# Kernel optimization log

Measured on AMD Instinct MI355X. Metric: run time of the kernel, lower is better.

## Reference

```python
import jax, jax.numpy as jnp
import numpy as np

D, H, L, P, NQ, B, DFF = 256, 8, 4, 4, 900, 4, 1024
SHAPES = [(128, 128), (64, 64), (32, 32), (16, 16)]
S = sum(h * w for h, w in SHAPES)  # 21760
HD = D // H


def setup_inputs() -> dict:
    key = jax.random.key(0)
    ks = iter(jax.random.split(key, 32))
    r = lambda sh, s=1.0: jax.random.normal(next(ks), sh, jnp.float32) * s
    return dict(
        tgt=r((B, NQ, D)),
        query_pos=r((B, NQ, D)),
        reference_points=jax.random.uniform(next(ks), (B, NQ, L, 2), jnp.float32),
        memory=r((B, S, D)),
        in_proj_w=r((D, 3 * D), 0.02), in_proj_b=jnp.zeros(3 * D, jnp.float32),
        out_proj_w=r((D, D), 0.02), out_proj_b=jnp.zeros(D, jnp.float32),
        ln1_g=jnp.ones(D, jnp.float32), ln1_b=jnp.zeros(D, jnp.float32),
        ln2_g=jnp.ones(D, jnp.float32), ln2_b=jnp.zeros(D, jnp.float32),
        ln3_g=jnp.ones(D, jnp.float32), ln3_b=jnp.zeros(D, jnp.float32),
        vproj_w=r((D, D), 0.02), vproj_b=jnp.zeros(D, jnp.float32),
        off_w=r((D, H * L * P * 2), 0.02), off_b=r((H * L * P * 2,), 0.5),
        aw_w=r((D, H * L * P), 0.02), aw_b=jnp.zeros(H * L * P, jnp.float32),
        oproj_w=r((D, D), 0.02), oproj_b=jnp.zeros(D, jnp.float32),
        lin1_w=r((D, DFF), 0.02), lin1_b=jnp.zeros(DFF, jnp.float32),
        lin2_w=r((DFF, D), 0.02), lin2_b=jnp.zeros(D, jnp.float32),
        spatial_shapes=np.array(SHAPES, np.int32),
        mem_mask=jnp.zeros((B, S), bool),
    )


def _ln(x, g, b):
    m = jnp.mean(x, -1, keepdims=True)
    v = jnp.mean((x - m) ** 2, -1, keepdims=True)
    return (x - m) * jax.lax.rsqrt(v + 1e-5) * g + b


def reference(tgt, query_pos, reference_points, memory,
              in_proj_w, in_proj_b, out_proj_w, out_proj_b,
              ln1_g, ln1_b, ln2_g, ln2_b, ln3_g, ln3_b,
              vproj_w, vproj_b, off_w, off_b, aw_w, aw_b, oproj_w, oproj_b,
              lin1_w, lin1_b, lin2_w, lin2_b, spatial_shapes, mem_mask):
    shapes = np.asarray(spatial_shapes)  # static level shapes

    # ---- self attention (nn.MultiheadAttention, q=k=tgt+pos, v=tgt) ----
    qp = tgt + query_pos
    q = qp @ in_proj_w[:, :D] + in_proj_b[:D]
    k = qp @ in_proj_w[:, D:2 * D] + in_proj_b[D:2 * D]
    v = tgt @ in_proj_w[:, 2 * D:] + in_proj_b[2 * D:]
    split = lambda x: x.reshape(B, NQ, H, HD).transpose(0, 2, 1, 3)
    qh, kh, vh = split(q), split(k), split(v)
    att = jax.nn.softmax(jnp.einsum('bhqd,bhkd->bhqk', qh, kh) / np.sqrt(HD).astype(np.float32), -1)
    sa = jnp.einsum('bhqk,bhkd->bhqd', att, vh).transpose(0, 2, 1, 3).reshape(B, NQ, D)
    tgt = _ln(tgt + sa @ out_proj_w + out_proj_b, ln2_g, ln2_b)

    # ---- MSDeformAttn cross attention ----
    query = tgt + query_pos
    value = memory @ vproj_w + vproj_b
    value = jnp.where(mem_mask[..., None], 0.0, value).reshape(B, S, H, HD)
    off = (query @ off_w + off_b).reshape(B, NQ, H, L, P, 2)
    aw = jax.nn.softmax((query @ aw_w + aw_b).reshape(B, NQ, H, L * P), -1).reshape(B, NQ, H, L, P)
    # offset normalizer is (W_l, H_l)
    normalizer = jnp.stack([jnp.asarray(shapes[:, 1]), jnp.asarray(shapes[:, 0])], -1).astype(jnp.float32)
    loc = reference_points[:, :, None, :, None, :] + off / normalizer[None, None, None, :, None, :]

    acc = jnp.zeros((B, NQ, H, HD), tgt.dtype)
    start = 0
    bidx = jnp.arange(B)[:, None, None, None]
    hidx = jnp.arange(H)[None, None, :, None]
    for l in range(L):
        Hl, Wl = int(shapes[l, 0]), int(shapes[l, 1])
        vf = value[:, start:start + Hl * Wl]  # [B, Hl*Wl, H, HD]
        # grid_sample align_corners=False, zero padding: pixel = loc*size - 0.5
        x = loc[:, :, :, l, :, 0] * Wl - 0.5  # [B,NQ,H,P]
        y = loc[:, :, :, l, :, 1] * Hl - 0.5
        x0 = jnp.floor(x); y0 = jnp.floor(y)
        wx = x - x0; wy = y - y0
        x0i = x0.astype(jnp.int32); y0i = y0.astype(jnp.int32)

        def gather(xi, yi):
            valid = (xi >= 0) & (xi < Wl) & (yi >= 0) & (yi < Hl)
            idx = jnp.clip(yi, 0, Hl - 1) * Wl + jnp.clip(xi, 0, Wl - 1)
            g = vf[bidx, idx, hidx]  # [B,NQ,H,P,HD]
            return jnp.where(valid[..., None], g, 0.0)

        samp = (gather(x0i, y0i) * ((1 - wx) * (1 - wy))[..., None]
                + gather(x0i + 1, y0i) * (wx * (1 - wy))[..., None]
                + gather(x0i, y0i + 1) * ((1 - wx) * wy)[..., None]
                + gather(x0i + 1, y0i + 1) * (wx * wy)[..., None])
        acc = acc + (samp * aw[:, :, :, l, :, None]).sum(3)
        start += Hl * Wl

    ca = acc.reshape(B, NQ, D) @ oproj_w + oproj_b
    tgt = _ln(tgt + ca, ln1_g, ln1_b)

    # ---- FFN ----
    ff = jax.nn.relu(tgt @ lin1_w + lin1_b) @ lin2_w + lin2_b
    return _ln(tgt + ff, ln3_g, ln3_b)
```

## Files before the change

kernel.cpp:

```cpp
#include <hip/hip_runtime.h>
#include <hip/hip_bf16.h>

typedef __attribute__((ext_vector_type(8))) short bf16x8;
typedef __attribute__((ext_vector_type(4))) short bf16x4;
typedef __attribute__((ext_vector_type(4))) float f32x4;

#define DEV static __device__ __forceinline__

constexpr int Bc = 4, NQc = 900, Hc = 8, Sc = 21760;
constexpr int M1 = Bc * NQc;
constexpr int NQT = (NQc + 63) / 64;
constexpr int QT16 = (NQc + 15) / 16;
constexpr int QKo = Bc * Hc * 960 * 32;

DEV short f2bf(float f) {
  union { __hip_bfloat16 h; short s; } u;
  u.h = __float2bfloat16(f);
  return u.s;
}
DEV float bf2f(short s) {
  union { short s; __hip_bfloat16 h; } u;
  u.s = s;
  return __bfloat162float(u.h);
}

DEV void pack_body(const float* W, short* Wt, int K, int N, int t) {
  int n = t % N;
  int k4 = (t / N) * 4;
  bf16x4 o;
  o[0] = f2bf(W[(size_t)(k4 + 0) * N + n]);
  o[1] = f2bf(W[(size_t)(k4 + 1) * N + n]);
  o[2] = f2bf(W[(size_t)(k4 + 2) * N + n]);
  o[3] = f2bf(W[(size_t)(k4 + 3) * N + n]);
  *(bf16x4*)&Wt[((size_t)(k4 >> 5) * N + n) * 32 + (k4 & 31)] = o;
}

__global__ __launch_bounds__(256) void pack_all_k(
    const float* w0, short* t0, const float* w1, short* t1,
    const float* w2, short* t2, const float* w3, short* t3,
    const float* w4, short* t4, const float* w5, short* t5) {
  int t = blockIdx.x * 256 + threadIdx.x;
  if (t < 49152) pack_body(w0, t0, 256, 768, t);
  else if (t < 65536) pack_body(w1, t1, 256, 256, t - 49152);
  else if (t < 81920) pack_body(w2, t2, 256, 256, t - 65536);
  else if (t < 98304) pack_body(w3, t3, 256, 256, t - 81920);
  else if (t < 163840) pack_body(w4, t4, 256, 1024, t - 98304);
  else pack_body(w5, t5, 1024, 256, t - 163840);
}

template <int MODE, int ACT, int MT>
__global__ __launch_bounds__(256) void gemmv_k(
    const float* __restrict__ A, const float* __restrict__ A2,
    const short* __restrict__ Wt, const float* __restrict__ bias,
    void* __restrict__ Cv, float* __restrict__ C2, int M, int N, int K,
    const unsigned char* __restrict__ rowmask, const float* __restrict__ g,
    const float* __restrict__ beta, const float* __restrict__ resid,
    const float* __restrict__ qpos, float* __restrict__ out2) {
  constexpr int IT = MT / 16;
  __shared__ short As[MT * 40];
  __shared__ short Ws[256 * 40];
  const int nb = N >> 8;
  const int mb = blockIdx.x / nb, bn = blockIdx.x - mb * nb;
  const int tid = threadIdx.x;
  const int lane = tid & 63, wave = tid >> 6;
  const int l16 = lane & 15, quad = lane >> 4;
  const int sr = (MT == 64) ? (tid >> 2) : (tid >> 3);
  const int sk = (MT == 64) ? ((tid & 3) * 8) : ((tid & 7) * 4);
  const int arow = mb * MT + sr;
  const bool aval = arow < M;
  const bool useA2 = (MODE == 4) ? (bn < 2) : (A2 != nullptr);
  const float* ap = A + (size_t)arow * K + sk;
  const float* ap2 = (A2 ? A2 : A) + (size_t)arow * K + sk;
  const short* wp = Wt + (size_t)(bn * 256 + tid) * 32;
  const size_t wstep = (size_t)N * 32;
  const int KT = K >> 5;

  f32x4 acc[IT][4] = {};
  float4 pa0[2] = {}, pa1[2] = {};
  bf16x8 pw[2][4];

  auto loadA = [&](int s, int it) {
    if (aval) {
      const float* p = ap + it * 32;
      pa0[s] = *(const float4*)p;
      if constexpr (MT == 64) pa1[s] = *(const float4*)(p + 4);
      if (useA2) {
        const float* p2 = ap2 + it * 32;
        float4 q0 = *(const float4*)p2;
        pa0[s].x += q0.x; pa0[s].y += q0.y; pa0[s].z += q0.z; pa0[s].w += q0.w;
        if constexpr (MT == 64) {
          float4 q1 = *(const float4*)(p2 + 4);
          pa1[s].x += q1.x; pa1[s].y += q1.y; pa1[s].z += q1.z; pa1[s].w += q1.w;
        }
      }
    }
  };
  auto loadW = [&](int s, int it) {
    const short* p = wp + (size_t)it * wstep;
    pw[s][0] = *(const bf16x8*)(p + 0);
    pw[s][1] = *(const bf16x8*)(p + 8);
    pw[s][2] = *(const bf16x8*)(p + 16);
    pw[s][3] = *(const bf16x8*)(p + 24);
  };
  auto stage = [&](int s) {
    if constexpr (MT == 64) {
      bf16x8 t;
      t[0] = f2bf(pa0[s].x); t[1] = f2bf(pa0[s].y); t[2] = f2bf(pa0[s].z); t[3] = f2bf(pa0[s].w);
      t[4] = f2bf(pa1[s].x); t[5] = f2bf(pa1[s].y); t[6] = f2bf(pa1[s].z); t[7] = f2bf(pa1[s].w);
      *(bf16x8*)&As[sr * 40 + sk] = t;
    } else {
      bf16x4 t;
      t[0] = f2bf(pa0[s].x); t[1] = f2bf(pa0[s].y); t[2] = f2bf(pa0[s].z); t[3] = f2bf(pa0[s].w);
      *(bf16x4*)&As[sr * 40 + sk] = t;
    }
    short* wd = &Ws[tid * 40];
    *(bf16x8*)(wd + 0) = pw[s][0];
    *(bf16x8*)(wd + 8) = pw[s][1];
    *(bf16x8*)(wd + 16) = pw[s][2];
    *(bf16x8*)(wd + 24) = pw[s][3];
  };
  auto compute = [&]() {
    bf16x8 af[IT], bfr[4];
#pragma unroll
    for (int i = 0; i < IT; i++)
      af[i] = *(const bf16x8*)&As[(i * 16 + l16) * 40 + quad * 8];
#pragma unroll
    for (int j = 0; j < 4; j++)
      bfr[j] = *(const bf16x8*)&Ws[(wave * 64 + j * 16 + l16) * 40 + quad * 8];
#pragma unroll
    for (int i = 0; i < IT; i++)
#pragma unroll
      for (int j = 0; j < 4; j++)
        acc[i][j] = __builtin_amdgcn_mfma_f32_16x16x32_bf16(af[i], bfr[j], acc[i][j], 0, 0, 0);
  };

  loadA(0, 0); loadW(0, 0);
  loadA(1, 1); loadW(1, 1);
  for (int it = 0; it < KT; it += 2) {
    stage(0);
    __syncthreads();
    if (it + 2 < KT) { loadA(0, it + 2); loadW(0, it + 2); }
    compute();
    __syncthreads();
    stage(1);
    __syncthreads();
    if (it + 3 < KT) { loadA(1, it + 3); loadW(1, it + 3); }
    compute();
    __syncthreads();
  }

  if constexpr (MODE == 4) {
    short* base = (short*)Cv;
#pragma unroll
    for (int i = 0; i < IT; i++)
#pragma unroll
      for (int r = 0; r < 4; r++) {
        const int m = mb * MT + i * 16 + quad * 4 + r;
        if (m >= M) continue;
        const int b = m / NQc, q = m - b * NQc;
#pragma unroll
        for (int j = 0; j < 4; j++) {
          const int cl = wave * 64 + j * 16 + l16;
          const float v = acc[i][j][r] + bias[bn * 256 + cl];
          const int h = cl >> 5, ch = cl & 31;
          if (bn == 0) {
            base[((size_t)(b * 8 + h) * 960 + q) * 32 + ch] =
                f2bf(v * 0.17677669529663687f);
          } else if (bn == 1) {
            base[QKo + ((size_t)(b * 8 + h) * 960 + q) * 32 + ch] = f2bf(v);
          } else {
            base[2 * QKo + ((((size_t)(b * 8 + h) * 15 + (q >> 6)) * 32 + ch) * 64 + (q & 63))] = f2bf(v);
          }
        }
      }
  } else if constexpr (MODE == 0) {
#pragma unroll
    for (int i = 0; i < IT; i++)
#pragma unroll
      for (int j = 0; j < 4; j++) {
        const int cl = wave * 64 + j * 16 + l16;
        const int col = bn * 256 + cl;
        const float bb = bias[col];
#pragma unroll
        for (int r = 0; r < 4; r++) {
          const int m = mb * MT + i * 16 + quad * 4 + r;
          if (m < M) {
            float v = acc[i][j][r] + bb;
            if (ACT == 1) v = fmaxf(v, 0.f);
            ((float*)Cv)[(size_t)m * N + col] = v;
          }
        }
      }
  } else {
#pragma unroll
    for (int j = 0; j < 4; j++) {
      const int cl = wave * 64 + j * 16 + l16;
      const float bb = bias[cl];
#pragma unroll
      for (int i = 0; i < IT; i++)
#pragma unroll
        for (int r = 0; r < 4; r++) {
          const int m = mb * MT + i * 16 + quad * 4 + r;
          const float rs = (m < M) ? resid[(size_t)m * 256 + cl] : 0.f;
          acc[i][j][r] += bb + rs;
        }
    }
    float2* pr = (float2*)As;
#pragma unroll
    for (int i = 0; i < IT; i++)
#pragma unroll
      for (int r = 0; r < 4; r++) {
        float s = 0.f, q = 0.f;
#pragma unroll
        for (int j = 0; j < 4; j++) {
          s += acc[i][j][r];
          q += acc[i][j][r] * acc[i][j][r];
        }
#pragma unroll
        for (int d = 1; d < 16; d <<= 1) {
          s += __shfl_xor(s, d);
          q += __shfl_xor(q, d);
        }
        if (l16 == 0) pr[(i * 16 + quad * 4 + r) * 4 + wave] = make_float2(s, q);
      }
    __syncthreads();
#pragma unroll
    for (int i = 0; i < IT; i++)
#pragma unroll
      for (int r = 0; r < 4; r++) {
        const int ml = i * 16 + quad * 4 + r;
        float2 p0 = pr[ml * 4 + 0], p1 = pr[ml * 4 + 1];
        float2 p2 = pr[ml * 4 + 2], p3 = pr[ml * 4 + 3];
        const float sum = p0.x + p1.x + p2.x + p3.x;
        const float sq = p0.y + p1.y + p2.y + p3.y;
        const float mean = sum * (1.f / 256.f);
        const float var = sq * (1.f / 256.f) - mean * mean;
        const float rstd = rsqrtf(var + 1e-5f);
        const int m = mb * MT + ml;
        if (m < M) {
#pragma unroll
          for (int j = 0; j < 4; j++) {
            const int cl = wave * 64 + j * 16 + l16;
            const float o = (acc[i][j][r] - mean) * rstd * g[cl] + beta[cl];
            ((float*)Cv)[(size_t)m * 256 + cl] = o;
            if (out2) out2[(size_t)m * 256 + cl] = o + qpos[(size_t)m * 256 + cl];
          }
        }
      }
  }
}

__global__ __launch_bounds__(256) void gemm_val_k(
    const float* __restrict__ A, const short* __restrict__ Wt,
    const float* __restrict__ bias, short* __restrict__ Cv, int M,
    const unsigned char* __restrict__ rowmask) {
  __shared__ short As[128 * 40];
  __shared__ short Ws[256 * 40];
  const int mb = blockIdx.x;
  const int tid = threadIdx.x;
  const int lane = tid & 63, wave = tid >> 6;
  const int l16 = lane & 15, quad = lane >> 4;
  const int sr = tid >> 1, sk = (tid & 1) * 16;
  const int arow = mb * 128 + sr;
  const bool aval = arow < M;
  const float* ap = A + (size_t)arow * 256 + sk;
  const short* wp = Wt + (size_t)tid * 32;

  f32x4 acc[8][4] = {};
  float4 pa[4];
  bf16x8 pwr[4];

  auto loadA = [&](int it) {
    if (aval) {
#pragma unroll
      for (int i = 0; i < 4; i++) pa[i] = *(const float4*)(ap + it * 32 + i * 4);
    }
  };
  auto loadW = [&](int it) {
    const short* p = wp + (size_t)it * (256 * 32);
    pwr[0] = *(const bf16x8*)(p + 0);
    pwr[1] = *(const bf16x8*)(p + 8);
    pwr[2] = *(const bf16x8*)(p + 16);
    pwr[3] = *(const bf16x8*)(p + 24);
  };

  loadA(0); loadW(0);
  for (int it = 0; it < 8; ++it) {
    {
      bf16x8 t0, t1;
      t0[0] = f2bf(pa[0].x); t0[1] = f2bf(pa[0].y); t0[2] = f2bf(pa[0].z); t0[3] = f2bf(pa[0].w);
      t0[4] = f2bf(pa[1].x); t0[5] = f2bf(pa[1].y); t0[6] = f2bf(pa[1].z); t0[7] = f2bf(pa[1].w);
      t1[0] = f2bf(pa[2].x); t1[1] = f2bf(pa[2].y); t1[2] = f2bf(pa[2].z); t1[3] = f2bf(pa[2].w);
      t1[4] = f2bf(pa[3].x); t1[5] = f2bf(pa[3].y); t1[6] = f2bf(pa[3].z); t1[7] = f2bf(pa[3].w);
      *(bf16x8*)&As[sr * 40 + sk] = t0;
      *(bf16x8*)&As[sr * 40 + sk + 8] = t1;
      short* wd = &Ws[tid * 40];
      *(bf16x8*)(wd + 0) = pwr[0];
      *(bf16x8*)(wd + 8) = pwr[1];
      *(bf16x8*)(wd + 16) = pwr[2];
      *(bf16x8*)(wd + 24) = pwr[3];
    }
    __syncthreads();
    if (it + 1 < 8) { loadA(it + 1); loadW(it + 1); }
    bf16x8 af[8], bfr[4];
#pragma unroll
    for (int i = 0; i < 8; i++)
      af[i] = *(const bf16x8*)&As[(i * 16 + l16) * 40 + quad * 8];
#pragma unroll
    for (int j = 0; j < 4; j++)
      bfr[j] = *(const bf16x8*)&Ws[(wave * 64 + j * 16 + l16) * 40 + quad * 8];
#pragma unroll
    for (int i = 0; i < 8; i++)
#pragma unroll
      for (int j = 0; j < 4; j++)
        acc[i][j] = __builtin_amdgcn_mfma_f32_16x16x32_bf16(af[i], bfr[j], acc[i][j], 0, 0, 0);
    __syncthreads();
  }
#pragma unroll
  for (int i = 0; i < 8; i++)
#pragma unroll
    for (int j = 0; j < 4; j++) {
      const int cl = wave * 64 + j * 16 + l16;
      const float bb = bias[cl];
#pragma unroll
      for (int r = 0; r < 4; r++) {
        const int m = mb * 128 + i * 16 + quad * 4 + r;
        if (m < M) {
          float v = acc[i][j][r] + bb;
          if (rowmask[m]) v = 0.f;
          Cv[(size_t)m * 256 + cl] = f2bf(v);
        }
      }
    }
}

DEV void gemm32_body(const float* __restrict__ A, const float* __restrict__ W,
                     const float* __restrict__ bias, float* __restrict__ C,
                     int M, int N, int K, int bid) {
  __shared__ float Asf[16][64];
  __shared__ float Bsf[16][68];
  const int nb = N >> 6;
  const int bm = bid / nb, bn = bid % nb;
  const int tid = threadIdx.x;
  const int tm = tid >> 4, tn = tid & 15;
  float acc[4][4] = {};

  for (int k0 = 0; k0 < K; k0 += 16) {
    {
      const int m = tid >> 2, kk = (tid & 3) * 4;
      const int row = bm * 64 + m;
      float4 v = (row < M) ? *(const float4*)(A + (size_t)row * K + k0 + kk)
                           : make_float4(0.f, 0.f, 0.f, 0.f);
      Asf[kk + 0][m] = v.x; Asf[kk + 1][m] = v.y;
      Asf[kk + 2][m] = v.z; Asf[kk + 3][m] = v.w;
    }
    {
      const int kk = tid >> 4, n = (tid & 15) * 4;
      float4 v = *(const float4*)(W + (size_t)(k0 + kk) * N + bn * 64 + n);
      *(float4*)&Bsf[kk][n] = v;
    }
    __syncthreads();
#pragma unroll
    for (int kk = 0; kk < 16; kk++) {
      float a[4], b[4];
#pragma unroll
      for (int i = 0; i < 4; i++) a[i] = Asf[kk][tm * 4 + i];
#pragma unroll
      for (int j = 0; j < 4; j++) b[j] = Bsf[kk][tn * 4 + j];
#pragma unroll
      for (int i = 0; i < 4; i++)
#pragma unroll
        for (int j = 0; j < 4; j++) acc[i][j] = fmaf(a[i], b[j], acc[i][j]);
    }
    __syncthreads();
  }
#pragma unroll
  for (int i = 0; i < 4; i++) {
    const int row = bm * 64 + tm * 4 + i;
    if (row >= M) continue;
#pragma unroll
    for (int j = 0; j < 4; j++) {
      const int col = bn * 64 + tn * 4 + j;
      C[(size_t)row * N + col] = acc[i][j] + bias[col];
    }
  }
}

__global__ __launch_bounds__(256) void gemm32_offaw_k(
    const float* __restrict__ query, const float* __restrict__ off_w,
    const float* __restrict__ off_b, float* __restrict__ offb,
    const float* __restrict__ aw_w, const float* __restrict__ aw_b,
    float* __restrict__ awlin) {
  if (blockIdx.x < 228)
    gemm32_body(query, off_w, off_b, offb, M1, 256, 256, blockIdx.x);
  else
    gemm32_body(query, aw_w, aw_b, awlin, M1, 128, 256, blockIdx.x - 228);
}

__global__ __launch_bounds__(128) void attn_k(const short* __restrict__ qbf,
                                              const short* __restrict__ kbf,
                                              const short* __restrict__ vtbf,
                                              float* __restrict__ sa) {
  __shared__ short Pb[2][16 * 72];
  __shared__ float Om[2][16][32];
  __shared__ float Ml[2][16][2];
  const int bid = blockIdx.x;
  const int qt = bid % QT16, bh = bid / QT16;
  const int tid = threadIdx.x, lane = tid & 63, wave = tid >> 6;
  const int l16 = lane & 15, quad = lane >> 4;

  const int q_local = min(qt * 16 + l16, NQc - 1);
  const bf16x8 qf = *(const bf16x8*)&qbf[((size_t)bh * 960 + q_local) * 32 + quad * 8];
  const short* kb = kbf + (size_t)bh * 960 * 32;
  const short* vb = vtbf + (size_t)bh * 15 * 32 * 64;

  f32x4 o0 = {}, o1 = {};
  float mrun[4] = {-1e30f, -1e30f, -1e30f, -1e30f};
  float lrun[4] = {0.f, 0.f, 0.f, 0.f};
  short* pw = Pb[wave];

  for (int kt = wave; kt < NQT; kt += 2) {
    const int k0 = kt * 64;
    f32x4 s[4];
#pragma unroll
    for (int st = 0; st < 4; st++) {
      const int key = k0 + st * 16 + l16;
      const bf16x8 kf = *(const bf16x8*)&kb[(size_t)key * 32 + quad * 8];
      f32x4 z = {};
      s[st] = __builtin_amdgcn_mfma_f32_16x16x32_bf16(qf, kf, z, 0, 0, 0);
      if (key >= NQc) { s[st][0] = -1e30f; s[st][1] = -1e30f; s[st][2] = -1e30f; s[st][3] = -1e30f; }
    }
    float mnew[4], alpha[4];
#pragma unroll
    for (int r = 0; r < 4; r++) {
      float mx = fmaxf(fmaxf(s[0][r], s[1][r]), fmaxf(s[2][r], s[3][r]));
#pragma unroll
      for (int d = 1; d < 16; d <<= 1) mx = fmaxf(mx, __shfl_xor(mx, d));
      mnew[r] = fmaxf(mrun[r], mx);
      alpha[r] = __expf(mrun[r] - mnew[r]);
      mrun[r] = mnew[r];
    }
    float tsum[4] = {0.f, 0.f, 0.f, 0.f};
#pragma unroll
    for (int st = 0; st < 4; st++)
#pragma unroll
      for (int r = 0; r < 4; r++) {
        float p = __expf(s[st][r] - mnew[r]);
        s[st][r] = p;
        tsum[r] += p;
      }
#pragma unroll
    for (int r = 0; r < 4; r++) {
      float t = tsum[r];
#pragma unroll
      for (int d = 1; d < 16; d <<= 1) t += __shfl_xor(t, d);
      lrun[r] = lrun[r] * alpha[r] + t;
      o0[r] *= alpha[r];
      o1[r] *= alpha[r];
    }
#pragma unroll
    for (int st = 0; st < 4; st++)
#pragma unroll
      for (int r = 0; r < 4; r++)
        pw[(quad * 4 + r) * 72 + st * 16 + l16] = f2bf(s[st][r]);
    const short* vt = vb + kt * (32 * 64);
#pragma unroll
    for (int c = 0; c < 2; c++) {
      bf16x8 pf = *(const bf16x8*)&pw[l16 * 72 + c * 32 + quad * 8];
      bf16x8 vf0 = *(const bf16x8*)&vt[(size_t)l16 * 64 + c * 32 + quad * 8];
      bf16x8 vf1 = *(const bf16x8*)&vt[(size_t)(16 + l16) * 64 + c * 32 + quad * 8];
      o0 = __builtin_amdgcn_mfma_f32_16x16x32_bf16(pf, vf0, o0, 0, 0, 0);
      o1 = __builtin_amdgcn_mfma_f32_16x16x32_bf16(pf, vf1, o1, 0, 0, 0);
    }
  }
#pragma unroll
  for (int r = 0; r < 4; r++) {
    Om[wave][quad * 4 + r][l16] = o0[r];
    Om[wave][quad * 4 + r][16 + l16] = o1[r];
  }
  if (l16 == 0) {
#pragma unroll
    for (int r = 0; r < 4; r++) {
      Ml[wave][quad * 4 + r][0] = mrun[r];
      Ml[wave][quad * 4 + r][1] = lrun[r];
    }
  }
  __syncthreads();
  {
    const int q = tid >> 3;
    const int c4 = (tid & 7) * 4;
    const float m0 = Ml[0][q][0], m1 = Ml[1][q][0];
    const float M = fmaxf(m0, m1);
    const float a0 = __expf(m0 - M), a1 = __expf(m1 - M);
    const float lsum = a0 * Ml[0][q][1] + a1 * Ml[1][q][1];
    const int qg = qt * 16 + q;
    if (qg < NQc) {
      const float inv = 1.f / lsum;
      float4 o;
      o.x = (a0 * Om[0][q][c4 + 0] + a1 * Om[1][q][c4 + 0]) * inv;
      o.y = (a0 * Om[0][q][c4 + 1] + a1 * Om[1][q][c4 + 1]) * inv;
      o.z = (a0 * Om[0][q][c4 + 2] + a1 * Om[1][q][c4 + 2]) * inv;
      o.w = (a0 * Om[0][q][c4 + 3] + a1 * Om[1][q][c4 + 3]) * inv;
      const int b = bh >> 3, h = bh & 7;
      *(float4*)&sa[(size_t)(b * NQc + qg) * 256 + h * 32 + c4] = o;
    }
  }
}

__global__ __launch_bounds__(256) void sample_k(
    const float* __restrict__ awlin, const float* __restrict__ off,
    const float* __restrict__ refp, const short* __restrict__ value,
    float* __restrict__ accout) {
  const int wid = blockIdx.x * 4 + (threadIdx.x >> 6);
  const int lane = threadIdx.x & 63;
  const int bq = wid >> 3, h = wid & 7;
  const int b = bq / NQc;
  const int l16 = lane & 15;

  float wraw = awlin[(size_t)bq * 128 + h * 16 + l16];
  float mx = wraw;
#pragma unroll
  for (int d = 1; d < 16; d <<= 1) mx = fmaxf(mx, __shfl_xor(mx, d));
  float e = __expf(wraw - mx), ssum = e;
#pragma unroll
  for (int d = 1; d < 16; d <<= 1) ssum += __shfl_xor(ssum, d);
  const float wnorm = e / ssum;

  const int ch = lane & 31, sub = lane >> 5;
  float facc = 0.f;
#pragma unroll
  for (int it = 0; it < 8; it++) {
    const int pt = it * 2 + sub;
    const float w = __shfl(wnorm, pt);
    const int l = pt >> 2;
    const int W = 128 >> l;
    const int start = (l == 0) ? 0 : (l == 1) ? 16384 : (l == 2) ? 20480 : 21504;
    const float offx = off[(size_t)bq * 256 + h * 32 + pt * 2];
    const float offy = off[(size_t)bq * 256 + h * 32 + pt * 2 + 1];
    const float rx = refp[(size_t)bq * 8 + l * 2];
    const float ry = refp[(size_t)bq * 8 + l * 2 + 1];
    const float x = rx * (float)W + offx - 0.5f;
    const float y = ry * (float)W + offy - 0.5f;
    const float x0f = floorf(x), y0f = floorf(y);
    const float wx = x - x0f, wy = y - y0f;
    const int x0 = (int)x0f, y0 = (int)y0f;
    const short* vbp = value + ((size_t)b * Sc + start) * 256 + h * 32 + ch;
#pragma unroll
    for (int c4 = 0; c4 < 4; c4++) {
      const int dx = c4 & 1, dy = c4 >> 1;
      const int xi = x0 + dx, yi = y0 + dy;
      const bool valid = (xi >= 0) && (xi < W) && (yi >= 0) && (yi < W);
      const int xc = min(max(xi, 0), W - 1);
      const int yc = min(max(yi, 0), W - 1);
      const float gvv = bf2f(vbp[(size_t)(yc * W + xc) * 256]);
      const float ww = (dx ? wx : 1.f - wx) * (dy ? wy : 1.f - wy);
      facc += valid ? w * ww * gvv : 0.f;
    }
  }
  facc += __shfl_xor(facc, 32);
  if (lane < 32) accout[(size_t)bq * 256 + h * 32 + ch] = facc;
}

extern "C" void kernel_launch(void* const* d_in, const int* in_sizes, int n_in,
                              void* d_out, int out_size, void* d_ws,
                              size_t ws_size, hipStream_t stream) {
  const float* tgt = (const float*)d_in[0];
  const float* query_pos = (const float*)d_in[1];
  const float* refp = (const float*)d_in[2];
  const float* memory = (const float*)d_in[3];
  const float* in_proj_w = (const float*)d_in[4];
  const float* in_proj_b = (const float*)d_in[5];
  const float* out_proj_w = (const float*)d_in[6];
  const float* out_proj_b = (const float*)d_in[7];
  const float* ln1_g = (const float*)d_in[8];
  const float* ln1_b = (const float*)d_in[9];
  const float* ln2_g = (const float*)d_in[10];
  const float* ln2_b = (const float*)d_in[11];
  const float* ln3_g = (const float*)d_in[12];
  const float* ln3_b = (const float*)d_in[13];
  const float* vproj_w = (const float*)d_in[14];
  const float* vproj_b = (const float*)d_in[15];
  const float* off_w = (const float*)d_in[16];
  const float* off_b = (const float*)d_in[17];
  const float* aw_w = (const float*)d_in[18];
  const float* aw_b = (const float*)d_in[19];
  const float* oproj_w = (const float*)d_in[20];
  const float* oproj_b = (const float*)d_in[21];
  const float* lin1_w = (const float*)d_in[22];
  const float* lin1_b = (const float*)d_in[23];
  const float* lin2_w = (const float*)d_in[24];
  const float* lin2_b = (const float*)d_in[25];
  const unsigned char* mem_mask = (const unsigned char*)d_in[27];
  float* out = (float*)d_out;

  float* ws = (float*)d_ws;
  short* qbf = (short*)(ws + 921600);
  float* sa = ws + 3686400;
  float* tgt2 = ws + 5529600;
  float* query = ws + 6451200;
  float* offb = ws + 7372800;
  float* awlin = ws + 8294400;
  float* accb = ws + 8755200;
  float* tgt3 = ws + 9676800;
  float* ff1 = ws + 10598400;
  short* valueBf = (short*)(ws + 14284800);
  short* wbase = valueBf + 22282240;
  short* inT = wbase + 0;
  short* outT = wbase + 196608;
  short* vT = wbase + 262144;
  short* oT = wbase + 327680;
  short* lin1T = wbase + 393216;
  short* lin2T = wbase + 655360;

  pack_all_k<<<896, 256, 0, stream>>>(in_proj_w, inT, out_proj_w, outT,
                                      vproj_w, vT, oproj_w, oT,
                                      lin1_w, lin1T, lin2_w, lin2T);

  gemmv_k<4, 0, 32><<<113 * 3, 256, 0, stream>>>(
      tgt, query_pos, inT, in_proj_b, qbf, nullptr, M1, 768, 256,
      nullptr, nullptr, nullptr, nullptr, nullptr, nullptr);
  attn_k<<<Bc * Hc * QT16, 128, 0, stream>>>(qbf, qbf + QKo, qbf + 2 * QKo, sa);
  gemmv_k<3, 0, 32><<<113, 256, 0, stream>>>(
      sa, nullptr, outT, out_proj_b, tgt2, nullptr, M1, 256, 256,
      nullptr, ln2_g, ln2_b, tgt, query_pos, query);
  gemm_val_k<<<680, 256, 0, stream>>>(memory, vT, vproj_b, valueBf, Bc * Sc, mem_mask);
  gemm32_offaw_k<<<342, 256, 0, stream>>>(query, off_w, off_b, offb, aw_w, aw_b, awlin);
  sample_k<<<Bc * NQc * Hc / 4, 256, 0, stream>>>(awlin, offb, refp, valueBf, accb);
  gemmv_k<3, 0, 32><<<113, 256, 0, stream>>>(
      accb, nullptr, oT, oproj_b, tgt3, nullptr, M1, 256, 256,
      nullptr, ln1_g, ln1_b, tgt2, nullptr, nullptr);
  gemmv_k<0, 1, 64><<<57 * 4, 256, 0, stream>>>(
      tgt3, nullptr, lin1T, lin1_b, ff1, nullptr, M1, 1024, 256,
      nullptr, nullptr, nullptr, nullptr, nullptr, nullptr);
  gemmv_k<3, 0, 32><<<113, 256, 0, stream>>>(
      ff1, nullptr, lin2T, lin2_b, out, nullptr, M1, 256, 1024,
      nullptr, ln3_g, ln3_b, tgt3, nullptr, nullptr);
}
```

Measured before the change: 429.3 us.

## Drop LDS staging in value-projection GEMM, load fragments directly from global

The value-projection GEMM no longer stages A and W tiles through shared memory with barriers. Each lane loads its MFMA fragments straight from global memory into a double-buffered register pipeline. The M tile shrinks from 128 to 64 rows, doubling the grid to 1360 blocks. This removes the LDS round trips and syncthreads. In exchange the four waves now reread the same A rows from global memory or cache, and the accesses are less coalesced. The rows-in-range guard on A loads is also dropped, which relies on M dividing evenly by 64 (87040 does).

```diff
diff --git a/kernel.cpp b/kernel.cpp
--- a/kernel.cpp
+++ b/kernel.cpp
@@ -254,82 +254,77 @@
     const float* __restrict__ A, const short* __restrict__ Wt,
     const float* __restrict__ bias, short* __restrict__ Cv, int M,
     const unsigned char* __restrict__ rowmask) {
-  __shared__ short As[128 * 40];
-  __shared__ short Ws[256 * 40];
   const int mb = blockIdx.x;
   const int tid = threadIdx.x;
   const int lane = tid & 63, wave = tid >> 6;
   const int l16 = lane & 15, quad = lane >> 4;
-  const int sr = tid >> 1, sk = (tid & 1) * 16;
-  const int arow = mb * 128 + sr;
-  const bool aval = arow < M;
-  const float* ap = A + (size_t)arow * 256 + sk;
-  const short* wp = Wt + (size_t)tid * 32;
-
-  f32x4 acc[8][4] = {};
-  float4 pa[4];
-  bf16x8 pwr[4];
-
-  auto loadA = [&](int it) {
-    if (aval) {
-#pragma unroll
-      for (int i = 0; i < 4; i++) pa[i] = *(const float4*)(ap + it * 32 + i * 4);
+
+  const float* ap = A + (size_t)(mb * 64 + l16) * 256 + quad * 8;
+  const short* wp = Wt + (size_t)(wave * 64 + l16) * 32 + quad * 8;
+
+  f32x4 acc[4][4] = {};
+  float4 pa[2][4][2];
+  bf16x8 pb[2][4];
+
+  auto loadA = [&](int s, int it) {
+#pragma unroll
+    for (int i = 0; i < 4; i++) {
+      const float* p = ap + (size_t)i * (16 * 256) + it * 32;
+      pa[s][i][0] = *(const float4*)p;
+      pa[s][i][1] = *(const float4*)(p + 4);
     }
   };
-  auto loadW = [&](int it) {
-    const short* p = wp + (size_t)it * (256 * 32);
-    pwr[0] = *(const bf16x8*)(p + 0);
-    pwr[1] = *(const bf16x8*)(p + 8);
-    pwr[2] = *(const bf16x8*)(p + 16);
-    pwr[3] = *(const bf16x8*)(p + 24);
+  auto loadB = [&](int s, int it) {
+#pragma unroll
+    for (int j = 0; j < 4; j++)
+      pb[s][j] = *(const bf16x8*)(wp + (size_t)(it * 256 + j * 16) * 32);
   };
-
-  loadA(0); loadW(0);
-  for (int it = 0; it < 8; ++it) {
-    {
-      bf16x8 t0, t1;
-      t0[0] = f2bf(pa[0].x); t0[1] = f2bf(pa[0].y); t0[2] = f2bf(pa[0].z); t0[3] = f2bf(pa[0].w);
-      t0[4] = f2bf(pa[1].x); t0[5] = f2bf(pa[1].y); t0[6] = f2bf(pa[1].z); t0[7] = f2bf(pa[1].w);
-      t1[0] = f2bf(pa[2].x); t1[1] = f2bf(pa[2].y); t1[2] = f2bf(pa[2].z); t1[3] = f2bf(pa[2].w);
-      t1[4] = f2bf(pa[3].x); t1[5] = f2bf(pa[3].y); t1[6] = f2bf(pa[3].z); t1[7] = f2bf(pa[3].w);
-      *(bf16x8*)&As[sr * 40 + sk] = t0;
-      *(bf16x8*)&As[sr * 40 + sk + 8] = t1;
-      short* wd = &Ws[tid * 40];
-      *(bf16x8*)(wd + 0) = pwr[0];
-      *(bf16x8*)(wd + 8) = pwr[1];
-      *(bf16x8*)(wd + 16) = pwr[2];
-      *(bf16x8*)(wd + 24) = pwr[3];
-    }
-    __syncthreads();
-    if (it + 1 < 8) { loadA(it + 1); loadW(it + 1); }
-    bf16x8 af[8], bfr[4];
-#pragma unroll
-    for (int i = 0; i < 8; i++)
-      af[i] = *(const bf16x8*)&As[(i * 16 + l16) * 40 + quad * 8];
-#pragma unroll
-    for (int j = 0; j < 4; j++)
-      bfr[j] = *(const bf16x8*)&Ws[(wave * 64 + j * 16 + l16) * 40 + quad * 8];
-#pragma unroll
-    for (int i = 0; i < 8; i++)
+  auto comp = [&](int s) {
+    bf16x8 af[4];
+#pragma unroll
+    for (int i = 0; i < 4; i++) {
+      af[i][0] = f2bf(pa[s][i][0].x);
+      af[i][1] = f2bf(pa[s][i][0].y);
+      af[i][2] = f2bf(pa[s][i][0].z);
+      af[i][3] = f2bf(pa[s][i][0].w);
+      af[i][4] = f2bf(pa[s][i][1].x);
+      af[i][5] = f2bf(pa[s][i][1].y);
+      af[i][6] = f2bf(pa[s][i][1].z);
+      af[i][7] = f2bf(pa[s][i][1].w);
+    }
+#pragma unroll
+    for (int i = 0; i < 4; i++)
 #pragma unroll
       for (int j = 0; j < 4; j++)
-        acc[i][j] = __builtin_amdgcn_mfma_f32_16x16x32_bf16(af[i], bfr[j], acc[i][j], 0, 0, 0);
-    __syncthreads();
-  }
-#pragma unroll
-  for (int i = 0; i < 8; i++)
-#pragma unroll
-    for (int j = 0; j < 4; j++) {
-      const int cl = wave * 64 + j * 16 + l16;
-      const float bb = bias[cl];
-#pragma unroll
-      for (int r = 0; r < 4; r++) {
-        const int m = mb * 128 + i * 16 + quad * 4 + r;
-        if (m < M) {
-          float v = acc[i][j][r] + bb;
-          if (rowmask[m]) v = 0.f;
-          Cv[(size_t)m * 256 + cl] = f2bf(v);
-        }
+        acc[i][j] = __builtin_amdgcn_mfma_f32_16x16x32_bf16(af[i], pb[s][j], acc[i][j], 0, 0, 0);
+  };
+
+  loadA(0, 0); loadB(0, 0);
+  loadA(1, 1); loadB(1, 1);
+#pragma unroll
+  for (int it = 0; it < 8; it += 2) {
+    comp(0);
+    if (it + 2 < 8) { loadA(0, it + 2); loadB(0, it + 2); }
+    comp(1);
+    if (it + 3 < 8) { loadA(1, it + 3); loadB(1, it + 3); }
+  }
+
+  float bb[4];
+#pragma unroll
+  for (int j = 0; j < 4; j++) bb[j] = bias[wave * 64 + j * 16 + l16];
+#pragma unroll
+  for (int i = 0; i < 4; i++)
+#pragma unroll
+    for (int r = 0; r < 4; r++) {
+      const int m = mb * 64 + i * 16 + quad * 4 + r;
+      if (m >= M) continue;
+      const bool mk = rowmask[m] != 0;
+#pragma unroll
+      for (int j = 0; j < 4; j++) {
+        const int cl = wave * 64 + j * 16 + l16;
+        float v = acc[i][j][r] + bb[j];
+        if (mk) v = 0.f;
+        Cv[(size_t)m * 256 + cl] = f2bf(v);
       }
     }
 }
@@ -623,7 +618,7 @@
   gemmv_k<3, 0, 32><<<113, 256, 0, stream>>>(
       sa, nullptr, outT, out_proj_b, tgt2, nullptr, M1, 256, 256,
       nullptr, ln2_g, ln2_b, tgt, query_pos, query);
-  gemm_val_k<<<680, 256, 0, stream>>>(memory, vT, vproj_b, valueBf, Bc * Sc, mem_mask);
+  gemm_val_k<<<1360, 256, 0, stream>>>(memory, vT, vproj_b, valueBf, Bc * Sc, mem_mask);
   gemm32_offaw_k<<<342, 256, 0, stream>>>(query, off_w, off_b, offb, aw_w, aw_b, awlin);
   sample_k<<<Bc * NQc * Hc / 4, 256, 0, stream>>>(awlin, offb, refp, valueBf, accb);
   gemmv_k<3, 0, 32><<<113, 256, 0, stream>>>(
```

New measurement: 422.7 us. Within noise of the previous version (-1.5%).
